# Kernel optimization log

Measured on AMD Instinct MI355X. Metric: run time of the kernel, lower is better.

Reference implementation:

```python
import jax, jax.numpy as jnp
import numpy as np

B, NQ, S, D = 8, 1024, 2048, 512

def setup_inputs() -> dict:
    key = jax.random.key(0)
    k1, k2, k3, k4 = jax.random.split(key, 4)
    queries = jax.random.normal(k1, (B, NQ, D), dtype=jnp.float32)
    keys = jax.random.normal(k2, (B, S, D), dtype=jnp.float32)
    values = jax.random.normal(k3, (B, S, D), dtype=jnp.float32)
    mask = jax.random.randint(k4, (B, NQ, S), 0, 2, dtype=jnp.int32)
    return {"queries": queries, "keys": keys, "values": values, "mask": mask}

def reference(queries, keys, values, mask):
    # scores: dot-product attention scores (b, nq, s)
    scores = jnp.einsum('bqd,bsd->bqs', queries, keys)
    attention_dist = jax.nn.softmax(scores, axis=2)
    # mask then renormalize over seq axis
    attention_dist = attention_dist * mask.astype(attention_dist.dtype)
    attention_dist = attention_dist / attention_dist.sum(axis=2, keepdims=True)
    # weighted sum of values: equivalent to (dist.unsqueeze(3) * values.unsqueeze(1)).sum(2)
    final_vector = jnp.einsum('bqs,bsd->bqd', attention_dist, values)
    return final_vector
```

## Files before the change

### kernel.cpp

```cpp
#include <hip/hip_runtime.h>


#define Bz 8
#define NQz 1024
#define Sz 2048
#define Dz 512
#define QTT 64
#define TS 32
#define KP 520
#define PP 40

typedef _Float16 f16x8 __attribute__((ext_vector_type(8)));
typedef float f32x4 __attribute__((ext_vector_type(4)));
typedef unsigned short ushort_t;

#define AS1(p) ((const __attribute__((address_space(1))) unsigned int*)(p))
#define AS3(p) ((__attribute__((address_space(3))) unsigned int*)(p))
#define DRAIN_ALL() __builtin_amdgcn_s_waitcnt(0)
#define DRAIN_BAR()                                         \
  do {                                                      \
    asm volatile("s_waitcnt vmcnt(0)" ::: "memory");        \
    __builtin_amdgcn_s_barrier();                           \
    asm volatile("" ::: "memory");                          \
  } while (0)

__device__ __forceinline__ ushort_t f2h(float x) {
  _Float16 h = (_Float16)x;
  return __builtin_bit_cast(ushort_t, h);
}
__device__ __forceinline__ float h2f(ushort_t u) {
  return (float)__builtin_bit_cast(_Float16, u);
}

__global__ __launch_bounds__(256)
void prep(const float* __restrict__ K, const float* __restrict__ V,
          const int* __restrict__ Mi, ushort_t* __restrict__ Kf,
          ushort_t* __restrict__ Vt, unsigned* __restrict__ Mp) {
  __shared__ ushort_t sT[64][41];
  const int t = threadIdx.x;
  int bx = blockIdx.x;
  if (bx < 8192) {
    size_t e = ((size_t)bx * 256 + t) * 4;
    float4 v = *(const float4*)(K + e);
    uint2 w;
    w.x = (unsigned)f2h(v.x) | ((unsigned)f2h(v.y) << 16);
    w.y = (unsigned)f2h(v.z) | ((unsigned)f2h(v.w) << 16);
    *(uint2*)(Kf + e) = w;
    return;
  }
  bx -= 8192;
  if (bx < 4096) {
    const int b = bx >> 9;
    const int rest = bx & 511;
    const int st = rest >> 4;
    const int dt = rest & 15;
    const int s0 = st * 64, d0 = dt * 32;
    const float* Vb = V + ((size_t)b * Sz + s0) * Dz + d0;
#pragma unroll
    for (int i = 0; i < 2; ++i) {
      int idx = t + 256 * i;
      int s = idx >> 3;
      int dc = (idx & 7) * 4;
      float4 v = *(const float4*)(Vb + (size_t)s * Dz + dc);
      uint2 w;
      w.x = (unsigned)f2h(v.x) | ((unsigned)f2h(v.y) << 16);
      w.y = (unsigned)f2h(v.z) | ((unsigned)f2h(v.w) << 16);
      *(uint2*)(&sT[s][dc]) = w;
    }
    __syncthreads();
    ushort_t* VtB = Vt + ((size_t)b * Dz + d0) * Sz + s0;
    int d = t >> 3, c = t & 7;
    uint4 u;
    ushort_t* tp = (ushort_t*)&u;
#pragma unroll
    for (int j = 0; j < 8; ++j) tp[j] = sT[c * 8 + j][d];
    *(uint4*)(VtB + (size_t)d * Sz + c * 8) = u;
    return;
  }
  bx -= 4096;
  const int lane = t & 63;
  const size_t base = (size_t)bx * 1024 + t * 4;
  const int4 mv = *(const int4*)(Mi + base);
  unsigned nib = (mv.x ? 1u : 0u) | (mv.y ? 2u : 0u) |
                 (mv.z ? 4u : 0u) | (mv.w ? 8u : 0u);
  unsigned v = nib << ((lane & 7) * 4);
  v |= __shfl_xor(v, 1);
  v |= __shfl_xor(v, 2);
  v |= __shfl_xor(v, 4);
  if ((lane & 7) == 0) Mp[bx * 32 + (t >> 3)] = v;
}

template <int SPLIT>
__global__ __launch_bounds__(256, 2)
void attn_flash(const float* __restrict__ Q, const unsigned* __restrict__ Mp,
                const ushort_t* __restrict__ Kf, const ushort_t* __restrict__ Vt,
                ushort_t* __restrict__ Opart, float* __restrict__ Mpart,
                float* __restrict__ Lpart) {
  __shared__ ushort_t sK[TS][KP];
  __shared__ ushort_t sV[Dz][TS];
  __shared__ ushort_t sP[4][16][PP];

  const int tid  = threadIdx.x;
  const int wave = tid >> 6;
  const int lane = tid & 63;
  const int l16  = lane & 15;
  const int quad = lane >> 4;

  const int bxr = blockIdx.x;
  const int b   = bxr & 7;
  const int rest = bxr >> 3;
  const int qt  = rest / SPLIT;
  const int sh  = rest % SPLIT;
  const int q0  = qt * QTT;
  const int SLEN = Sz / SPLIT;
  const int NTt  = SLEN / TS;
  const int sbeg = sh * SLEN;
  const int qw   = q0 + wave * 16;

  const float*    Qb  = Q  + ((size_t)b * NQz + qw) * Dz;
  const ushort_t* KfB = Kf + (size_t)b * Sz * Dz;
  const ushort_t* VtB = Vt + (size_t)b * Dz * Sz;
  const unsigned* MpB = Mp + ((size_t)b * NQz + qw) * (Sz / 32);

  const int vql  = (lane & 3) ^ ((lane >> 3) & 3);
  const int vcol = (quad ^ ((l16 >> 1) & 3)) * 8;

  auto issue_k = [&](int s0n) {
#pragma unroll
    for (int j = 0; j < 8; ++j) {
      int row = wave * 8 + j;
      const ushort_t* gp = KfB + (size_t)(s0n + row) * Dz + lane * 8;
      __builtin_amdgcn_global_load_lds(AS1(gp), AS3(&sK[row][0]), 16, 0, 0);
    }
  };
  auto issue_v = [&](int s0n) {
#pragma unroll
    for (int j = 0; j < 8; ++j) {
      int dbase = wave * 128 + j * 16;
      int d = dbase + (lane >> 2);
      const ushort_t* gp = VtB + (size_t)d * Sz + s0n + vql * 8;
      __builtin_amdgcn_global_load_lds(AS1(gp), AS3(&sV[dbase][0]), 16, 0, 0);
    }
  };

  issue_k(sbeg);
  issue_v(sbeg);
  unsigned msk_cur = MpB[(size_t)l16 * (Sz / 32) + (sbeg >> 5)];

  f16x8 qa[16];
  {
    const float* qrow = Qb + (size_t)l16 * Dz;
#pragma unroll
    for (int kk = 0; kk < 16; ++kk) {
      const float4 a = *(const float4*)(qrow + kk * 32 + quad * 8);
      const float4 c = *(const float4*)(qrow + kk * 32 + quad * 8 + 4);
      f16x8 h;
      h[0] = (_Float16)a.x; h[1] = (_Float16)a.y;
      h[2] = (_Float16)a.z; h[3] = (_Float16)a.w;
      h[4] = (_Float16)c.x; h[5] = (_Float16)c.y;
      h[6] = (_Float16)c.z; h[7] = (_Float16)c.w;
      qa[kk] = h;
    }
  }
  DRAIN_ALL();
  __syncthreads();

  float m_ln = -1e30f, l_ln = 0.0f;
  f32x4 oacc[32];
#pragma unroll
  for (int nt = 0; nt < 32; ++nt) oacc[nt] = (f32x4){0.f, 0.f, 0.f, 0.f};

  for (int i = 0; i < NTt; ++i) {
    f32x4 a00 = (f32x4){0.f,0.f,0.f,0.f}, a01 = (f32x4){0.f,0.f,0.f,0.f};
    f32x4 a10 = (f32x4){0.f,0.f,0.f,0.f}, a11 = (f32x4){0.f,0.f,0.f,0.f};
    {
      const ushort_t* kh0 = &sK[l16][quad * 8];
      const ushort_t* kh1 = &sK[16 + l16][quad * 8];
      __builtin_amdgcn_s_setprio(1);
#pragma unroll
      for (int kk = 0; kk < 16; kk += 2) {
        f16x8 k00 = *(const f16x8*)(kh0 + kk * 32);
        f16x8 k10 = *(const f16x8*)(kh1 + kk * 32);
        f16x8 k01 = *(const f16x8*)(kh0 + kk * 32 + 32);
        f16x8 k11 = *(const f16x8*)(kh1 + kk * 32 + 32);
        a00 = __builtin_amdgcn_mfma_f32_16x16x32_f16(k00, qa[kk], a00, 0, 0, 0);
        a10 = __builtin_amdgcn_mfma_f32_16x16x32_f16(k10, qa[kk], a10, 0, 0, 0);
        a01 = __builtin_amdgcn_mfma_f32_16x16x32_f16(k01, qa[kk+1], a01, 0, 0, 0);
        a11 = __builtin_amdgcn_mfma_f32_16x16x32_f16(k11, qa[kk+1], a11, 0, 0, 0);
      }
      __builtin_amdgcn_s_setprio(0);
    }
    f32x4 s0v, s1v;
#pragma unroll
    for (int r = 0; r < 4; ++r) { s0v[r] = a00[r] + a01[r]; s1v[r] = a10[r] + a11[r]; }

    const unsigned mb = msk_cur;
    float se0[4], se1[4];
#pragma unroll
    for (int r = 0; r < 4; ++r) {
      se0[r] = ((mb >> (quad * 4 + r)) & 1u)      ? s0v[r] : -1e30f;
      se1[r] = ((mb >> (16 + quad * 4 + r)) & 1u) ? s1v[r] : -1e30f;
    }
    float rmax = fmaxf(fmaxf(fmaxf(se0[0], se0[1]), fmaxf(se0[2], se0[3])),
                       fmaxf(fmaxf(se1[0], se1[1]), fmaxf(se1[2], se1[3])));
    rmax = fmaxf(rmax, __shfl_xor(rmax, 16));
    rmax = fmaxf(rmax, __shfl_xor(rmax, 32));

    ushort_t pb0[4], pb1[4];
    float rsum = 0.f;
#pragma unroll
    for (int r = 0; r < 4; ++r) {
      float p0 = ((mb >> (quad * 4 + r)) & 1u)      ? __expf(se0[r] - rmax) : 0.f;
      float p1 = ((mb >> (16 + quad * 4 + r)) & 1u) ? __expf(se1[r] - rmax) : 0.f;
      pb0[r] = f2h(p0); pb1[r] = f2h(p1);
      rsum += h2f(pb0[r]) + h2f(pb1[r]);
    }
    {
      uint2 w0, w1;
      w0.x = (unsigned)pb0[0] | ((unsigned)pb0[1] << 16);
      w0.y = (unsigned)pb0[2] | ((unsigned)pb0[3] << 16);
      w1.x = (unsigned)pb1[0] | ((unsigned)pb1[1] << 16);
      w1.y = (unsigned)pb1[2] | ((unsigned)pb1[3] << 16);
      *(uint2*)(&sP[wave][l16][quad * 4]) = w0;
      *(uint2*)(&sP[wave][l16][16 + quad * 4]) = w1;
    }
    rsum += __shfl_xor(rsum, 16);
    rsum += __shfl_xor(rsum, 32);

    float m_new = fmaxf(m_ln, rmax);
    float scl   = __expf(rmax - m_new);
    float al_ln = __expf(m_ln - m_new);
    bool  grw   = m_new > m_ln;
    l_ln = al_ln * l_ln + scl * rsum;
    m_ln = m_new;

    DRAIN_BAR();
    unsigned msk_nxt = 0;
    if (i + 1 < NTt) {
      msk_nxt = MpB[(size_t)l16 * (Sz / 32) + ((sbeg + (i + 1) * TS) >> 5)];
      issue_k(sbeg + (i + 1) * TS);
    }

    f16x8 praw = *(const f16x8*)(&sP[wave][l16][quad * 8]);
    f16x8 pa;
    {
      _Float16 sh16 = (_Float16)scl;
#pragma unroll
      for (int j = 0; j < 8; ++j) pa[j] = praw[j] * sh16;
    }

    if (__any((int)grw)) {
      float alr[4];
#pragma unroll
      for (int r = 0; r < 4; ++r) alr[r] = __shfl(al_ln, quad * 4 + r);
#pragma unroll
      for (int nt = 0; nt < 32; ++nt)
#pragma unroll
        for (int r = 0; r < 4; ++r) oacc[nt][r] *= alr[r];
    }

    {
      const ushort_t* vb_ = &sV[0][0] + (size_t)l16 * TS + vcol;
      __builtin_amdgcn_s_setprio(1);
#pragma unroll
      for (int nt = 0; nt < 32; ++nt) {
        f16x8 vb = *(const f16x8*)(vb_ + nt * 512);
        oacc[nt] = __builtin_amdgcn_mfma_f32_16x16x32_f16(pa, vb, oacc[nt], 0, 0, 0);
      }
      __builtin_amdgcn_s_setprio(0);
    }

    DRAIN_BAR();
    if (i + 1 < NTt) issue_v(sbeg + (i + 1) * TS);

    msk_cur = msk_nxt;
  }

  const size_t rbase = (size_t)(b * SPLIT + sh) * NQz + q0 + wave * 16;
#pragma unroll
  for (int nt = 0; nt < 32; ++nt) {
#pragma unroll
    for (int r = 0; r < 4; ++r) {
      Opart[(rbase + quad * 4 + r) * Dz + nt * 16 + l16] = f2h(oacc[nt][r]);
    }
  }
  if (quad == 0) {
    Mpart[rbase + l16] = m_ln;
    Lpart[rbase + l16] = l_ln;
  }
}

template <int SPLIT>
__global__ __launch_bounds__(256)
void combine(const ushort_t* __restrict__ Opart, const float* __restrict__ Mpart,
             const float* __restrict__ Lpart, float* __restrict__ Out) {
  int gid = blockIdx.x * 256 + threadIdx.x;
  int row = gid >> 7;
  int b   = row >> 10;
  int q   = row & 1023;
  int c   = (gid & 127) * 4;
  float mv[SPLIT], lv[SPLIT];
  float m = -1e30f;
#pragma unroll
  for (int p = 0; p < SPLIT; ++p) {
    size_t ip = (size_t)(b * SPLIT + p) * NQz + q;
    mv[p] = Mpart[ip];
    lv[p] = Lpart[ip];
    m = fmaxf(m, mv[p]);
  }
  float w[SPLIT], denom = 0.f;
#pragma unroll
  for (int p = 0; p < SPLIT; ++p) {
    w[p] = __expf(mv[p] - m);
    denom += w[p] * lv[p];
  }
  float inv = 1.0f / denom;
  float4 o = {0.f, 0.f, 0.f, 0.f};
#pragma unroll
  for (int p = 0; p < SPLIT; ++p) {
    size_t ip = (size_t)(b * SPLIT + p) * NQz + q;
    const ushort_t* op = Opart + ip * Dz + c;
    uint2 raw = *(const uint2*)op;
    o.x += w[p] * h2f((ushort_t)(raw.x & 0xffff));
    o.y += w[p] * h2f((ushort_t)(raw.x >> 16));
    o.z += w[p] * h2f((ushort_t)(raw.y & 0xffff));
    o.w += w[p] * h2f((ushort_t)(raw.y >> 16));
  }
  o.x *= inv; o.y *= inv; o.z *= inv; o.w *= inv;
  *(float4*)(Out + ((size_t)b * NQz + q) * Dz + c) = o;
}

extern "C" void kernel_launch(void* const* d_in, const int* in_sizes, int n_in,
                              void* d_out, int out_size, void* d_ws, size_t ws_size,
                              hipStream_t stream) {
  const float* Q = (const float*)d_in[0];
  const float* K = (const float*)d_in[1];
  const float* V = (const float*)d_in[2];
  const int*   M = (const int*)d_in[3];
  float* O = (float*)d_out;

  const size_t NKV   = (size_t)Bz * Sz * Dz;
  const size_t maskW = (size_t)Bz * NQz * (Sz / 32);

  ushort_t* Kf = (ushort_t*)d_ws;
  ushort_t* Vt = Kf + NKV;
  unsigned* Mp = (unsigned*)(Vt + NKV);
  ushort_t* Opart = (ushort_t*)(Mp + maskW);

  auto need_bytes = [&](int S) -> size_t {
    return NKV * 2 * 2 + maskW * 4
         + (size_t)Bz * S * NQz * Dz * 2
         + (size_t)Bz * S * NQz * 4 * 2;
  };

  prep<<<dim3(28672), dim3(256), 0, stream>>>(K, V, M, Kf, Vt, Mp);

  if (ws_size >= need_bytes(4)) {
    constexpr int S = 4;
    float* Mpart = (float*)(Opart + (size_t)Bz * S * NQz * Dz);
    float* Lpart = Mpart + (size_t)Bz * S * NQz;
    attn_flash<S><<<dim3(8 * (NQz / QTT) * S), dim3(256), 0, stream>>>(
        Q, Mp, Kf, Vt, Opart, Mpart, Lpart);
    combine<S><<<dim3(4096), dim3(256), 0, stream>>>(Opart, Mpart, Lpart, O);
  } else {
    constexpr int S = 2;
    float* Mpart = (float*)(Opart + (size_t)Bz * S * NQz * Dz);
    float* Lpart = Mpart + (size_t)Bz * S * NQz;
    attn_flash<S><<<dim3(8 * (NQz / QTT) * S), dim3(256), 0, stream>>>(
        Q, Mp, Kf, Vt, Opart, Mpart, Lpart);
    combine<S><<<dim3(4096), dim3(256), 0, stream>>>(Opart, Mpart, Lpart, O);
  }
}
```

Measured before the change: 248.6 us.

## Split head dim across blocks, shuffle P in registers, coarsen prep blocks

The attention kernel now splits the 512-wide value dimension into two halves across separate blocks. Each block keeps only 16 output accumulators and half the V tile in LDS, which allows three blocks per CU instead of two. The P tile is moved into the MFMA operand layout with cross-lane shuffles rather than a round-trip through shared memory. The QK score accumulation uses two accumulators instead of four. The prep kernel processes four chunks per block for K conversion and mask packing, and the sequence split is fixed at 2. The costs are that QK^T and the softmax are recomputed by both halves, and the extra shuffles lengthen the dependency chain.

```diff
diff --git a/kernel.cpp b/kernel.cpp
--- a/kernel.cpp
+++ b/kernel.cpp
@@ -8,7 +8,6 @@
 #define QTT 64
 #define TS 32
 #define KP 520
-#define PP 40
 
 typedef _Float16 f16x8 __attribute__((ext_vector_type(8)));
 typedef float f32x4 __attribute__((ext_vector_type(4)));
@@ -39,16 +38,20 @@
   __shared__ ushort_t sT[64][41];
   const int t = threadIdx.x;
   int bx = blockIdx.x;
-  if (bx < 8192) {
-    size_t e = ((size_t)bx * 256 + t) * 4;
-    float4 v = *(const float4*)(K + e);
-    uint2 w;
-    w.x = (unsigned)f2h(v.x) | ((unsigned)f2h(v.y) << 16);
-    w.y = (unsigned)f2h(v.z) | ((unsigned)f2h(v.w) << 16);
-    *(uint2*)(Kf + e) = w;
+  if (bx < 2048) {
+    const size_t base = (size_t)bx * 4096 + t * 4;
+#pragma unroll
+    for (int i = 0; i < 4; ++i) {
+      size_t e = base + i * 1024;
+      float4 v = *(const float4*)(K + e);
+      uint2 w;
+      w.x = (unsigned)f2h(v.x) | ((unsigned)f2h(v.y) << 16);
+      w.y = (unsigned)f2h(v.z) | ((unsigned)f2h(v.w) << 16);
+      *(uint2*)(Kf + e) = w;
+    }
     return;
   }
-  bx -= 8192;
+  bx -= 2048;
   if (bx < 4096) {
     const int b = bx >> 9;
     const int rest = bx & 511;
@@ -79,26 +82,28 @@
   }
   bx -= 4096;
   const int lane = t & 63;
-  const size_t base = (size_t)bx * 1024 + t * 4;
-  const int4 mv = *(const int4*)(Mi + base);
-  unsigned nib = (mv.x ? 1u : 0u) | (mv.y ? 2u : 0u) |
-                 (mv.z ? 4u : 0u) | (mv.w ? 8u : 0u);
-  unsigned v = nib << ((lane & 7) * 4);
-  v |= __shfl_xor(v, 1);
-  v |= __shfl_xor(v, 2);
-  v |= __shfl_xor(v, 4);
-  if ((lane & 7) == 0) Mp[bx * 32 + (t >> 3)] = v;
+#pragma unroll
+  for (int i = 0; i < 4; ++i) {
+    const size_t base = (size_t)bx * 4096 + i * 1024 + t * 4;
+    const int4 mv = *(const int4*)(Mi + base);
+    unsigned nib = (mv.x ? 1u : 0u) | (mv.y ? 2u : 0u) |
+                   (mv.z ? 4u : 0u) | (mv.w ? 8u : 0u);
+    unsigned v = nib << ((lane & 7) * 4);
+    v |= __shfl_xor(v, 1);
+    v |= __shfl_xor(v, 2);
+    v |= __shfl_xor(v, 4);
+    if ((lane & 7) == 0) Mp[bx * 128 + i * 32 + (t >> 3)] = v;
+  }
 }
 
 template <int SPLIT>
-__global__ __launch_bounds__(256, 2)
+__global__ __launch_bounds__(256, 3)
 void attn_flash(const float* __restrict__ Q, const unsigned* __restrict__ Mp,
                 const ushort_t* __restrict__ Kf, const ushort_t* __restrict__ Vt,
                 ushort_t* __restrict__ Opart, float* __restrict__ Mpart,
                 float* __restrict__ Lpart) {
   __shared__ ushort_t sK[TS][KP];
-  __shared__ ushort_t sV[Dz][TS];
-  __shared__ ushort_t sP[4][16][PP];
+  __shared__ ushort_t sV[256][TS];
 
   const int tid  = threadIdx.x;
   const int wave = tid >> 6;
@@ -109,9 +114,12 @@
   const int bxr = blockIdx.x;
   const int b   = bxr & 7;
   const int rest = bxr >> 3;
-  const int qt  = rest / SPLIT;
-  const int sh  = rest % SPLIT;
+  const int dh  = rest & 1;
+  const int r2  = rest >> 1;
+  const int sh  = r2 % SPLIT;
+  const int qt  = r2 / SPLIT;
   const int q0  = qt * QTT;
+  const int d0  = dh * 256;
   const int SLEN = Sz / SPLIT;
   const int NTt  = SLEN / TS;
   const int sbeg = sh * SLEN;
@@ -135,17 +143,20 @@
   };
   auto issue_v = [&](int s0n) {
 #pragma unroll
-    for (int j = 0; j < 8; ++j) {
-      int dbase = wave * 128 + j * 16;
-      int d = dbase + (lane >> 2);
+    for (int j = 0; j < 4; ++j) {
+      int dbase = wave * 64 + j * 16;
+      int d = d0 + dbase + (lane >> 2);
       const ushort_t* gp = VtB + (size_t)d * Sz + s0n + vql * 8;
       __builtin_amdgcn_global_load_lds(AS1(gp), AS3(&sV[dbase][0]), 16, 0, 0);
     }
   };
+  auto load_mask = [&](int s0n) -> unsigned {
+    return MpB[(size_t)l16 * (Sz / 32) + (s0n >> 5)];
+  };
 
   issue_k(sbeg);
   issue_v(sbeg);
-  unsigned msk_cur = MpB[(size_t)l16 * (Sz / 32) + (sbeg >> 5)];
+  unsigned msk_cur = load_mask(sbeg);
 
   f16x8 qa[16];
   {
@@ -166,33 +177,26 @@
   __syncthreads();
 
   float m_ln = -1e30f, l_ln = 0.0f;
-  f32x4 oacc[32];
-#pragma unroll
-  for (int nt = 0; nt < 32; ++nt) oacc[nt] = (f32x4){0.f, 0.f, 0.f, 0.f};
+  f32x4 oacc[16];
+#pragma unroll
+  for (int nt = 0; nt < 16; ++nt) oacc[nt] = (f32x4){0.f, 0.f, 0.f, 0.f};
 
   for (int i = 0; i < NTt; ++i) {
-    f32x4 a00 = (f32x4){0.f,0.f,0.f,0.f}, a01 = (f32x4){0.f,0.f,0.f,0.f};
-    f32x4 a10 = (f32x4){0.f,0.f,0.f,0.f}, a11 = (f32x4){0.f,0.f,0.f,0.f};
+    f32x4 s0v = (f32x4){0.f, 0.f, 0.f, 0.f};
+    f32x4 s1v = (f32x4){0.f, 0.f, 0.f, 0.f};
     {
       const ushort_t* kh0 = &sK[l16][quad * 8];
       const ushort_t* kh1 = &sK[16 + l16][quad * 8];
       __builtin_amdgcn_s_setprio(1);
 #pragma unroll
-      for (int kk = 0; kk < 16; kk += 2) {
-        f16x8 k00 = *(const f16x8*)(kh0 + kk * 32);
-        f16x8 k10 = *(const f16x8*)(kh1 + kk * 32);
-        f16x8 k01 = *(const f16x8*)(kh0 + kk * 32 + 32);
-        f16x8 k11 = *(const f16x8*)(kh1 + kk * 32 + 32);
-        a00 = __builtin_amdgcn_mfma_f32_16x16x32_f16(k00, qa[kk], a00, 0, 0, 0);
-        a10 = __builtin_amdgcn_mfma_f32_16x16x32_f16(k10, qa[kk], a10, 0, 0, 0);
-        a01 = __builtin_amdgcn_mfma_f32_16x16x32_f16(k01, qa[kk+1], a01, 0, 0, 0);
-        a11 = __builtin_amdgcn_mfma_f32_16x16x32_f16(k11, qa[kk+1], a11, 0, 0, 0);
+      for (int kk = 0; kk < 16; ++kk) {
+        f16x8 k0 = *(const f16x8*)(kh0 + kk * 32);
+        f16x8 k1 = *(const f16x8*)(kh1 + kk * 32);
+        s0v = __builtin_amdgcn_mfma_f32_16x16x32_f16(k0, qa[kk], s0v, 0, 0, 0);
+        s1v = __builtin_amdgcn_mfma_f32_16x16x32_f16(k1, qa[kk], s1v, 0, 0, 0);
       }
       __builtin_amdgcn_s_setprio(0);
     }
-    f32x4 s0v, s1v;
-#pragma unroll
-    for (int r = 0; r < 4; ++r) { s0v[r] = a00[r] + a01[r]; s1v[r] = a10[r] + a11[r]; }
 
     const unsigned mb = msk_cur;
     float se0[4], se1[4];
@@ -214,15 +218,6 @@
       float p1 = ((mb >> (16 + quad * 4 + r)) & 1u) ? __expf(se1[r] - rmax) : 0.f;
       pb0[r] = f2h(p0); pb1[r] = f2h(p1);
       rsum += h2f(pb0[r]) + h2f(pb1[r]);
-    }
-    {
-      uint2 w0, w1;
-      w0.x = (unsigned)pb0[0] | ((unsigned)pb0[1] << 16);
-      w0.y = (unsigned)pb0[2] | ((unsigned)pb0[3] << 16);
-      w1.x = (unsigned)pb1[0] | ((unsigned)pb1[1] << 16);
-      w1.y = (unsigned)pb1[2] | ((unsigned)pb1[3] << 16);
-      *(uint2*)(&sP[wave][l16][quad * 4]) = w0;
-      *(uint2*)(&sP[wave][l16][16 + quad * 4]) = w1;
     }
     rsum += __shfl_xor(rsum, 16);
     rsum += __shfl_xor(rsum, 32);
@@ -234,19 +229,33 @@
     l_ln = al_ln * l_ln + scl * rsum;
     m_ln = m_new;
 
+    f16x8 pa;
+    {
+      unsigned u0a = (unsigned)pb0[0] | ((unsigned)pb0[1] << 16);
+      unsigned u0b = (unsigned)pb0[2] | ((unsigned)pb0[3] << 16);
+      unsigned u1a = (unsigned)pb1[0] | ((unsigned)pb1[1] << 16);
+      unsigned u1b = (unsigned)pb1[2] | ((unsigned)pb1[3] << 16);
+      const int sA = l16 + ((quad & 1) ? 32 : 0);
+      const int sB = sA + 16;
+      unsigned lo0 = __shfl((int)u0a, sA), lo1 = __shfl((int)u0b, sA);
+      unsigned lo2 = __shfl((int)u0a, sB), lo3 = __shfl((int)u0b, sB);
+      unsigned hi0 = __shfl((int)u1a, sA), hi1 = __shfl((int)u1b, sA);
+      unsigned hi2 = __shfl((int)u1a, sB), hi3 = __shfl((int)u1b, sB);
+      const bool hi = quad >= 2;
+      uint4 w;
+      w.x = hi ? hi0 : lo0;  w.y = hi ? hi1 : lo1;
+      w.z = hi ? hi2 : lo2;  w.w = hi ? hi3 : lo3;
+      f16x8 praw = __builtin_bit_cast(f16x8, w);
+      _Float16 sh16 = (_Float16)scl;
+#pragma unroll
+      for (int j = 0; j < 8; ++j) pa[j] = praw[j] * sh16;
+    }
+
     DRAIN_BAR();
     unsigned msk_nxt = 0;
     if (i + 1 < NTt) {
-      msk_nxt = MpB[(size_t)l16 * (Sz / 32) + ((sbeg + (i + 1) * TS) >> 5)];
+      msk_nxt = load_mask(sbeg + (i + 1) * TS);
       issue_k(sbeg + (i + 1) * TS);
-    }
-
-    f16x8 praw = *(const f16x8*)(&sP[wave][l16][quad * 8]);
-    f16x8 pa;
-    {
-      _Float16 sh16 = (_Float16)scl;
-#pragma unroll
-      for (int j = 0; j < 8; ++j) pa[j] = praw[j] * sh16;
     }
 
     if (__any((int)grw)) {
@@ -254,7 +263,7 @@
 #pragma unroll
       for (int r = 0; r < 4; ++r) alr[r] = __shfl(al_ln, quad * 4 + r);
 #pragma unroll
-      for (int nt = 0; nt < 32; ++nt)
+      for (int nt = 0; nt < 16; ++nt)
 #pragma unroll
         for (int r = 0; r < 4; ++r) oacc[nt][r] *= alr[r];
     }
@@ -263,7 +272,7 @@
       const ushort_t* vb_ = &sV[0][0] + (size_t)l16 * TS + vcol;
       __builtin_amdgcn_s_setprio(1);
 #pragma unroll
-      for (int nt = 0; nt < 32; ++nt) {
+      for (int nt = 0; nt < 16; ++nt) {
         f16x8 vb = *(const f16x8*)(vb_ + nt * 512);
         oacc[nt] = __builtin_amdgcn_mfma_f32_16x16x32_f16(pa, vb, oacc[nt], 0, 0, 0);
       }
@@ -278,13 +287,13 @@
 
   const size_t rbase = (size_t)(b * SPLIT + sh) * NQz + q0 + wave * 16;
 #pragma unroll
-  for (int nt = 0; nt < 32; ++nt) {
+  for (int nt = 0; nt < 16; ++nt) {
 #pragma unroll
     for (int r = 0; r < 4; ++r) {
-      Opart[(rbase + quad * 4 + r) * Dz + nt * 16 + l16] = f2h(oacc[nt][r]);
-    }
-  }
-  if (quad == 0) {
+      Opart[(rbase + quad * 4 + r) * Dz + d0 + nt * 16 + l16] = f2h(oacc[nt][r]);
+    }
+  }
+  if (dh == 0 && quad == 0) {
     Mpart[rbase + l16] = m_ln;
     Lpart[rbase + l16] = l_ln;
   }
@@ -347,27 +356,12 @@
   unsigned* Mp = (unsigned*)(Vt + NKV);
   ushort_t* Opart = (ushort_t*)(Mp + maskW);
 
-  auto need_bytes = [&](int S) -> size_t {
-    return NKV * 2 * 2 + maskW * 4
-         + (size_t)Bz * S * NQz * Dz * 2
-         + (size_t)Bz * S * NQz * 4 * 2;
-  };
-
-  prep<<<dim3(28672), dim3(256), 0, stream>>>(K, V, M, Kf, Vt, Mp);
-
-  if (ws_size >= need_bytes(4)) {
-    constexpr int S = 4;
-    float* Mpart = (float*)(Opart + (size_t)Bz * S * NQz * Dz);
-    float* Lpart = Mpart + (size_t)Bz * S * NQz;
-    attn_flash<S><<<dim3(8 * (NQz / QTT) * S), dim3(256), 0, stream>>>(
-        Q, Mp, Kf, Vt, Opart, Mpart, Lpart);
-    combine<S><<<dim3(4096), dim3(256), 0, stream>>>(Opart, Mpart, Lpart, O);
-  } else {
-    constexpr int S = 2;
-    float* Mpart = (float*)(Opart + (size_t)Bz * S * NQz * Dz);
-    float* Lpart = Mpart + (size_t)Bz * S * NQz;
-    attn_flash<S><<<dim3(8 * (NQz / QTT) * S), dim3(256), 0, stream>>>(
-        Q, Mp, Kf, Vt, Opart, Mpart, Lpart);
-    combine<S><<<dim3(4096), dim3(256), 0, stream>>>(Opart, Mpart, Lpart, O);
-  }
-}
+  constexpr int S = 2;
+  float* Mpart = (float*)(Opart + (size_t)Bz * S * NQz * Dz);
+  float* Lpart = Mpart + (size_t)Bz * S * NQz;
+
+  prep<<<dim3(10240), dim3(256), 0, stream>>>(K, V, M, Kf, Vt, Mp);
+  attn_flash<S><<<dim3(8 * (NQz / QTT) * S * 2), dim3(256), 0, stream>>>(
+      Q, Mp, Kf, Vt, Opart, Mpart, Lpart);
+  combine<S><<<dim3(4096), dim3(256), 0, stream>>>(Opart, Mpart, Lpart, O);
+}
```

After: 288.2 us. +15.9%, slower.
